# Performance work log

Hardware: AMD Instinct MI355X
Metric: run time of the kernel (lower is better)

The kernel has to match this reference:

```python
import jax, jax.numpy as jnp
import numpy as np

N = 50000
E = 800000
IN_CH = 256
HID = 64
HEADS = 8
OUT_CH = 16
NEG_SLOPE = 0.2


def _glorot(key, shape):
    fan_in, fan_out = shape[0], shape[-1]
    lim = float(np.sqrt(6.0 / (fan_in + fan_out)))
    return jax.random.uniform(key, shape, jnp.float32, -lim, lim)


def setup_inputs() -> dict:
    key = jax.random.key(0)
    ks = jax.random.split(key, 12)
    x = jax.random.normal(ks[0], (N, IN_CH), jnp.float32)
    edge_index = jax.random.randint(ks[1], (2, E), 0, N, jnp.int64)
    # layer 1: GATConv(256 -> 64, heads=8)
    W1 = _glorot(ks[2], (IN_CH, HEADS * HID))
    a_src1 = _glorot(ks[3], (HEADS, HID))
    a_dst1 = _glorot(ks[4], (HEADS, HID))
    b1 = jnp.zeros((HEADS * HID,), jnp.float32)
    # layer 2: GATConv(512 -> 16, heads=1, concat=False)
    W2 = _glorot(ks[5], (HEADS * HID, OUT_CH))
    a_src2 = _glorot(ks[6], (1, OUT_CH))
    a_dst2 = _glorot(ks[7], (1, OUT_CH))
    b2 = jnp.zeros((OUT_CH,), jnp.float32)
    return {"x": x, "edge_index": edge_index, "W1": W1, "a_src1": a_src1,
            "a_dst1": a_dst1, "b1": b1, "W2": W2, "a_src2": a_src2,
            "a_dst2": a_dst2, "b2": b2}


def _gat_conv(x, src, dst, W, a_src, a_dst, bias, heads, out_ch, concat):
    n = x.shape[0]
    h = (x @ W).reshape(n, heads, out_ch)            # [N,H,C]
    alpha_s = jnp.einsum('nhc,hc->nh', h, a_src)      # [N,H]
    alpha_d = jnp.einsum('nhc,hc->nh', h, a_dst)
    e = alpha_s[src] + alpha_d[dst]                   # [E,H]
    e = jnp.where(e > 0, e, NEG_SLOPE * e)            # leaky_relu
    # segment softmax over incoming edges of each dst node
    e_max = jax.ops.segment_max(e, dst, num_segments=n)
    e_max = jnp.where(jnp.isfinite(e_max), e_max, 0.0)
    p = jnp.exp(e - e_max[dst])                       # [E,H]
    denom = jax.ops.segment_sum(p, dst, num_segments=n)
    alpha = p / (denom[dst] + 1e-16)                  # [E,H]
    msg = h[src] * alpha[:, :, None]                  # [E,H,C]
    out = jax.ops.segment_sum(msg, dst, num_segments=n)  # [N,H,C]
    if concat:
        out = out.reshape(n, heads * out_ch)
    else:
        out = out.mean(axis=1)
    return out + bias


def reference(x, edge_index, W1, a_src1, a_dst1, b1, W2, a_src2, a_dst2, b2):
    n = x.shape[0]
    loops = jnp.arange(n, dtype=edge_index.dtype)
    ei = jnp.concatenate([edge_index, jnp.stack([loops, loops])], axis=1)
    src, dst = ei[0], ei[1]
    h = _gat_conv(x, src, dst, W1, a_src1, a_dst1, b1, HEADS, HID, True)
    h = jax.nn.elu(h)
    out = _gat_conv(h, src, dst, W2, a_src2, a_dst2, b2, 1, OUT_CH, False)
    return jax.nn.log_softmax(out, axis=-1)
```

## Files before the change

kernel.cpp:

```cpp
#include <hip/hip_runtime.h>
#include <math.h>

#define IN_CH 256
#define HID 64
#define HEADS 8
#define F1 512
#define OUT_CH 16
#define NEG 0.2f

typedef __attribute__((ext_vector_type(8))) short bf16x8;
typedef __attribute__((ext_vector_type(4))) float f32x4;
typedef __attribute__((ext_vector_type(2))) float f32x2;

__device__ __forceinline__ unsigned short f2bf(float f) {
  unsigned int u = __builtin_bit_cast(unsigned int, f);
  u += 0x7FFFu + ((u >> 16) & 1u);
  return (unsigned short)(u >> 16);
}
__device__ __forceinline__ void gld_lds16(const void* g, void* l) {
  __builtin_amdgcn_global_load_lds(
      (const __attribute__((address_space(1))) unsigned int*)g,
      (__attribute__((address_space(3))) unsigned int*)l, 16, 0, 0);
}


__global__ void prep_kernel(const int* __restrict__ ei, int E, int N,
                            int* counts,
                            const float* __restrict__ W1, unsigned short* __restrict__ W1R,
                            const float* __restrict__ W2, unsigned short* __restrict__ W2T) {
  int idx = blockIdx.x * blockDim.x + threadIdx.x;
  int ET = E + N;
  if (idx < ET) {
    int dst = (idx < E) ? ei[E + idx] : (idx - E);
    atomicAdd(&counts[dst], 1);
  }
  if (idx < F1 * IN_CH) {
    int n = idx >> 8, k = idx & 255;
    int r = (((k >> 5) * 4 + ((k >> 3) & 3)) * 512 + n) * 8 + (k & 7);
    W1R[r] = f2bf(W1[k * F1 + n]);
  }
  if (idx < OUT_CH * F1) {
    int n = idx >> 9, k = idx & 511;
    W2T[idx] = f2bf(W2[k * OUT_CH + n]);
  }
}


__global__ __launch_bounds__(1024) void scan_kernel(const int* __restrict__ counts,
                                                    int* __restrict__ offsets,
                                                    int* __restrict__ bsum,
                                                    int* bars, int n) {
  __shared__ int lds[1024];
  __shared__ int s_pre, s_tot;
  int nb = gridDim.x;
  int t = threadIdx.x;
  int i = blockIdx.x * 1024 + t;
  int v = (i < n) ? counts[i] : 0;
  lds[t] = v;
  __syncthreads();
  for (int off = 1; off < 1024; off <<= 1) {
    int u = (t >= off) ? lds[t - off] : 0;
    __syncthreads();
    lds[t] += u;
    __syncthreads();
  }
  int incl = lds[t];
  if (t == 1023) bsum[blockIdx.x] = incl;
  __syncthreads();
  if (t == 0) {
    __threadfence();
    atomicAdd(&bars[0], 1);
    while (atomicAdd(&bars[0], 0) < nb) __builtin_amdgcn_s_sleep(8);
  }
  __syncthreads();
  if (t < 64) {
    int bv = (t < nb) ? bsum[t] : 0;
    int vp = (t < (int)blockIdx.x) ? bv : 0;
    #pragma unroll
    for (int off = 1; off < 64; off <<= 1) {
      vp += __shfl_xor(vp, off);
      bv += __shfl_xor(bv, off);
    }
    if (t == 0) { s_pre = vp; s_tot = bv; }
  }
  __syncthreads();
  if (i < n) offsets[i] = s_pre + incl - v;
  if (blockIdx.x == 0 && t == 0) offsets[n] = s_tot;
}

__global__ void fill_kernel(const int* __restrict__ ei, int E, int N,
                            const int* __restrict__ offsets, int* cursor,
                            int* __restrict__ csr_src) {
  int e = blockIdx.x * blockDim.x + threadIdx.x;
  int ET = E + N;
  if (e >= ET) return;
  int src, dst;
  if (e < E) { src = ei[e]; dst = ei[E + e]; }
  else       { src = e - E; dst = e - E; }
  int pos = atomicAdd(&cursor[dst], 1);
  csr_src[offsets[dst] + pos] = src;
}


__global__ __launch_bounds__(512) void gemm1_mfma(const float* __restrict__ X,
                                                  const unsigned short* __restrict__ W1R,
                                                  const float* __restrict__ Asrc,
                                                  const float* __restrict__ Adst,
                                                  unsigned char* __restrict__ C,
                                                  float2* __restrict__ aad1, int M) {
  __shared__ __align__(16) short sB[4 * 512 * 8];
  int tid = threadIdx.x, w = tid >> 6, l = tid & 63;
  int wm = (w >> 2) * 32;
  int wn = (w & 3) * 128;
  int bm = blockIdx.x * 64;
  f32x4 acc[2][8];
  #pragma unroll
  for (int mi = 0; mi < 2; ++mi)
    #pragma unroll
    for (int nj = 0; nj < 8; ++nj) acc[mi][nj] = (f32x4){0.f, 0.f, 0.f, 0.f};
  int kslot = l >> 4;
  for (int kb = 0; kb < 8; ++kb) {
    __syncthreads();
    const unsigned short* src = W1R + kb * 16384;
    #pragma unroll
    for (int i = 0; i < 4; ++i)
      gld_lds16(src + (size_t)(i * 512 + tid) * 8, (char*)sB + (i * 512 + tid) * 16);
    bf16x8 af[2];
    int kbase = kb * 32 + kslot * 8;
    #pragma unroll
    for (int mi = 0; mi < 2; ++mi) {
      int r = bm + wm + mi * 16 + (l & 15);
      if (r >= M) r = M - 1;
      const float* ap = X + (size_t)r * IN_CH + kbase;
      float4 a0 = *(const float4*)ap;
      float4 a1 = *(const float4*)(ap + 4);
      unsigned int u0, u1, u2, u3;
      asm("v_cvt_pk_bf16_f32 %0, %1, %2" : "=v"(u0) : "v"(a0.x), "v"(a0.y));
      asm("v_cvt_pk_bf16_f32 %0, %1, %2" : "=v"(u1) : "v"(a0.z), "v"(a0.w));
      asm("v_cvt_pk_bf16_f32 %0, %1, %2" : "=v"(u2) : "v"(a1.x), "v"(a1.y));
      asm("v_cvt_pk_bf16_f32 %0, %1, %2" : "=v"(u3) : "v"(a1.z), "v"(a1.w));
      int4 pk = make_int4(u0, u1, u2, u3);
      af[mi] = __builtin_bit_cast(bf16x8, pk);
    }
    __syncthreads();
    #pragma unroll
    for (int nj = 0; nj < 8; ++nj) {
      int n = wn + nj * 16 + (l & 15);
      bf16x8 bf = *(const bf16x8*)&sB[(kslot * 512 + n) * 8];
      acc[0][nj] = __builtin_amdgcn_mfma_f32_16x16x32_bf16(af[0], bf, acc[0][nj], 0, 0, 0);
      acc[1][nj] = __builtin_amdgcn_mfma_f32_16x16x32_bf16(af[1], bf, acc[1][nj], 0, 0, 0);
    }
  }
  float asv[8], adv[8];
  #pragma unroll
  for (int nj = 0; nj < 8; ++nj) {
    int c = wn + nj * 16 + (l & 15);
    asv[nj] = Asrc[c]; adv[nj] = Adst[c];
  }
  int h0 = (w & 3) * 2;
  #pragma unroll
  for (int mi = 0; mi < 2; ++mi) {
    #pragma unroll
    for (int j = 0; j < 4; ++j) {
      int r = bm + wm + mi * 16 + (l >> 4) * 4 + j;
      bool ok = (r < M);
      if (ok) {
        #pragma unroll
        for (int njp = 0; njp < 4; ++njp) {
          int u = __builtin_amdgcn_cvt_pk_fp8_f32(acc[mi][2 * njp][j],
                                                  acc[mi][2 * njp + 1][j], 0, false);
          int c0 = wn + (2 * njp) * 16 + (l & 15);
          C[(size_t)r * F1 + c0]      = (unsigned char)u;
          C[(size_t)r * F1 + c0 + 16] = (unsigned char)(u >> 8);
        }
      }
      float sA = 0.f, dA = 0.f, sB2 = 0.f, dB2 = 0.f;
      #pragma unroll
      for (int nj = 0; nj < 4; ++nj) {
        float v = acc[mi][nj][j];
        sA += v * asv[nj]; dA += v * adv[nj];
      }
      #pragma unroll
      for (int nj = 4; nj < 8; ++nj) {
        float v = acc[mi][nj][j];
        sB2 += v * asv[nj]; dB2 += v * adv[nj];
      }
      #pragma unroll
      for (int off = 1; off < 16; off <<= 1) {
        sA += __shfl_xor(sA, off); dA += __shfl_xor(dA, off);
        sB2 += __shfl_xor(sB2, off); dB2 += __shfl_xor(dB2, off);
      }
      if (ok && (l & 15) == 0) {
        aad1[r * HEADS + h0]     = make_float2(sA, dA);
        aad1[r * HEADS + h0 + 1] = make_float2(sB2, dB2);
      }
    }
  }
}


__global__ __launch_bounds__(256) void aggr1_kernel(const uint2* __restrict__ h1q,
                                                    const float2* __restrict__ aad1,
                                                    const int* __restrict__ offsets,
                                                    const int* __restrict__ csr_src,
                                                    const float* __restrict__ b1,
                                                    uint4* __restrict__ out1v, int N) {
  int tid = threadIdx.x;
  int w = tid >> 6, l = tid & 63;
  int b = blockIdx.x;
  int nwg = gridDim.x;
  int q = nwg >> 3, r = nwg & 7;
  int xcd = b & 7, bi = b >> 3;
  int swz = (xcd < r) ? (xcd * (q + 1) + bi) : (r * (q + 1) + (xcd - r) * q + bi);
  int node = swz * 4 + w;
  if (node >= N) return;
  int beg = offsets[node], deg = offsets[node + 1] - beg;
  int he = l & 7;
  int hc = l >> 3;
  float adv = aad1[node * HEADS + he].y;
  float pden = 0.f;
  f32x2 acc2[4];
  #pragma unroll
  for (int i = 0; i < 4; ++i) acc2[i] = (f32x2){0.f, 0.f};
  int e = l >> 3;
  for (int c0 = 0; c0 < deg; c0 += 8) {
    int cnt = min(8, deg - c0);
    int s8 = 0;
    float p8 = 0.f;
    if (e < cnt) {
      s8 = csr_src[beg + c0 + e];
      float2 sd = aad1[s8 * HEADS + he];
      float ev = sd.x + adv;
      ev = (ev > 0.f) ? ev : NEG * ev;
      p8 = __expf(ev);
      pden += p8;
    }
    if (cnt == 8) {
      int ss[8]; float qq[8];
      #pragma unroll
      for (int j = 0; j < 8; ++j) {
        ss[j] = __shfl(s8, j * 8);
        qq[j] = __shfl(p8, j * 8 + hc);
      }
      uint2 v[8];
      #pragma unroll
      for (int j = 0; j < 8; ++j) v[j] = h1q[(size_t)ss[j] * 64 + l];
      #pragma unroll
      for (int j = 0; j < 8; ++j) {
        f32x2 p2 = (f32x2){qq[j], qq[j]};
        acc2[0] += p2 * __builtin_amdgcn_cvt_pk_f32_fp8(v[j].x, false);
        acc2[1] += p2 * __builtin_amdgcn_cvt_pk_f32_fp8(v[j].x, true);
        acc2[2] += p2 * __builtin_amdgcn_cvt_pk_f32_fp8(v[j].y, false);
        acc2[3] += p2 * __builtin_amdgcn_cvt_pk_f32_fp8(v[j].y, true);
      }
    } else {
      for (int j = 0; j < cnt; ++j) {
        int s = __shfl(s8, j * 8);
        float p = __shfl(p8, j * 8 + hc);
        uint2 v = h1q[(size_t)s * 64 + l];
        f32x2 p2 = (f32x2){p, p};
        acc2[0] += p2 * __builtin_amdgcn_cvt_pk_f32_fp8(v.x, false);
        acc2[1] += p2 * __builtin_amdgcn_cvt_pk_f32_fp8(v.x, true);
        acc2[2] += p2 * __builtin_amdgcn_cvt_pk_f32_fp8(v.y, false);
        acc2[3] += p2 * __builtin_amdgcn_cvt_pk_f32_fp8(v.y, true);
      }
    }
  }
  pden += __shfl_xor(pden, 8);
  pden += __shfl_xor(pden, 16);
  pden += __shfl_xor(pden, 32);
  float den = __shfl(pden, hc) + 1e-16f;
  float4 bv0 = *(const float4*)&b1[l * 8];
  float4 bv1 = *(const float4*)&b1[l * 8 + 4];
  float o[8];
  o[0] = acc2[0][0] / den + bv0.x; o[1] = acc2[0][1] / den + bv0.y;
  o[2] = acc2[1][0] / den + bv0.z; o[3] = acc2[1][1] / den + bv0.w;
  o[4] = acc2[2][0] / den + bv1.x; o[5] = acc2[2][1] / den + bv1.y;
  o[6] = acc2[3][0] / den + bv1.z; o[7] = acc2[3][1] / den + bv1.w;
  #pragma unroll
  for (int i = 0; i < 8; ++i) o[i] = (o[i] > 0.f) ? o[i] : expm1f(o[i]);
  uint4 ov;
  ov.x = (unsigned int)f2bf(o[0]) | ((unsigned int)f2bf(o[1]) << 16);
  ov.y = (unsigned int)f2bf(o[2]) | ((unsigned int)f2bf(o[3]) << 16);
  ov.z = (unsigned int)f2bf(o[4]) | ((unsigned int)f2bf(o[5]) << 16);
  ov.w = (unsigned int)f2bf(o[6]) | ((unsigned int)f2bf(o[7]) << 16);
  out1v[(size_t)node * 64 + l] = ov;
}


__global__ __launch_bounds__(256) void gemm2_mfma(const unsigned short* __restrict__ A,
                                                  const unsigned short* __restrict__ W2T,
                                                  const float* __restrict__ a_src2,
                                                  const float* __restrict__ a_dst2,
                                                  float* __restrict__ t2,
                                                  float2* __restrict__ aad2, int M) {
  __shared__ __align__(16) short sW[16 * 512];
  int tid = threadIdx.x, w = tid >> 6, l = tid & 63;
  for (int i = tid; i < 1024; i += 256) ((uint4*)sW)[i] = ((const uint4*)W2T)[i];
  __syncthreads();
  int bm = blockIdx.x * 128 + w * 32;
  f32x4 acc[2];
  acc[0] = (f32x4){0.f, 0.f, 0.f, 0.f};
  acc[1] = (f32x4){0.f, 0.f, 0.f, 0.f};
  int rl = l & 15;
  int koff = (l >> 4) * 8;
  int r0 = bm + rl;       if (r0 >= M) r0 = M - 1;
  int r1 = bm + 16 + rl;  if (r1 >= M) r1 = M - 1;
  const unsigned short* a0p = A + (size_t)r0 * F1 + koff;
  const unsigned short* a1p = A + (size_t)r1 * F1 + koff;
  #pragma unroll
  for (int k0 = 0; k0 < F1; k0 += 32) {
    bf16x8 bfv = *(const bf16x8*)&sW[rl * 512 + k0 + koff];
    bf16x8 af0 = *(const bf16x8*)(a0p + k0);
    bf16x8 af1 = *(const bf16x8*)(a1p + k0);
    acc[0] = __builtin_amdgcn_mfma_f32_16x16x32_bf16(af0, bfv, acc[0], 0, 0, 0);
    acc[1] = __builtin_amdgcn_mfma_f32_16x16x32_bf16(af1, bfv, acc[1], 0, 0, 0);
  }
  float asv = a_src2[rl], adv = a_dst2[rl];
  #pragma unroll
  for (int mi = 0; mi < 2; ++mi) {
    #pragma unroll
    for (int j = 0; j < 4; ++j) {
      int r = bm + mi * 16 + (l >> 4) * 4 + j;
      float val = acc[mi][j];
      float s = val * asv, d = val * adv;
      s += __shfl_xor(s, 1); s += __shfl_xor(s, 2); s += __shfl_xor(s, 4); s += __shfl_xor(s, 8);
      d += __shfl_xor(d, 1); d += __shfl_xor(d, 2); d += __shfl_xor(d, 4); d += __shfl_xor(d, 8);
      if (r < M) {
        t2[(size_t)r * OUT_CH + rl] = val;
        if (rl == 0) aad2[r] = make_float2(s, d);
      }
    }
  }
}


__global__ __launch_bounds__(256) void aggr2_kernel(const float* __restrict__ t2,
                                                    const float2* __restrict__ aad2,
                                                    const int* __restrict__ offsets,
                                                    const int* __restrict__ csr_src,
                                                    const float* __restrict__ b2,
                                                    float* __restrict__ out, int N) {
  int tid = threadIdx.x;
  int node = blockIdx.x * 4 + (tid >> 6);
  int lane = tid & 63;
  if (node >= N) return;
  int beg = offsets[node];
  int deg = offsets[node + 1] - beg;
  float ad = aad2[node].y;
  float acc = 0.f, den = 0.f;
  int eg = lane >> 4, c = lane & 15;
  for (int base = 0; base < deg; base += 8) {
    int j1 = base + eg;
    int j2 = base + 4 + eg;
    bool ok1 = j1 < deg, ok2 = j2 < deg;
    int s1 = csr_src[beg + (ok1 ? j1 : 0)];
    int s2 = csr_src[beg + (ok2 ? j2 : 0)];
    float2 m1 = aad2[s1];
    float2 m2 = aad2[s2];
    float t1v = t2[(size_t)s1 * OUT_CH + c];
    float t2v = t2[(size_t)s2 * OUT_CH + c];
    float e1 = m1.x + ad;
    e1 = (e1 > 0.f) ? e1 : NEG * e1;
    float p1 = ok1 ? __expf(e1) : 0.f;
    float e2 = m2.x + ad;
    e2 = (e2 > 0.f) ? e2 : NEG * e2;
    float p2 = ok2 ? __expf(e2) : 0.f;
    acc += p1 * t1v + p2 * t2v;
    if (c == 0) den += p1 + p2;
  }
  acc += __shfl_xor(acc, 16); acc += __shfl_xor(acc, 32);
  den += __shfl_xor(den, 16); den += __shfl_xor(den, 32);
  den = __shfl(den, 0);
  float val = acc / (den + 1e-16f) + b2[c];
  float mx = val;
  #pragma unroll
  for (int off = 1; off < 16; off <<= 1) mx = fmaxf(mx, __shfl_xor(mx, off));
  float ex = __expf(val - mx);
  float se = ex;
  #pragma unroll
  for (int off = 1; off < 16; off <<= 1) se += __shfl_xor(se, off);
  float ls = val - mx - logf(se);
  if (lane < 16) out[(size_t)node * OUT_CH + lane] = ls;
}


extern "C" void kernel_launch(void* const* d_in, const int* in_sizes, int n_in,
                              void* d_out, int out_size, void* d_ws, size_t ws_size,
                              hipStream_t stream) {
  const float* x      = (const float*)d_in[0];
  const int*   ei     = (const int*)d_in[1];
  const float* W1     = (const float*)d_in[2];
  const float* a_src1 = (const float*)d_in[3];
  const float* a_dst1 = (const float*)d_in[4];
  const float* b1     = (const float*)d_in[5];
  const float* W2     = (const float*)d_in[6];
  const float* a_src2 = (const float*)d_in[7];
  const float* a_dst2 = (const float*)d_in[8];
  const float* b2     = (const float*)d_in[9];
  float* out = (float*)d_out;

  int N = in_sizes[0] / IN_CH;
  int E = in_sizes[1] / 2;
  int ET = E + N;

  char* w = (char*)d_ws;
  auto alloc = [&](size_t bytes) -> void* {
    void* p = (void*)w;
    w += (bytes + 255) & ~(size_t)255;
    return p;
  };
  unsigned char*  h1b   = (unsigned char*)alloc((size_t)N * F1);
  unsigned short* out1b = (unsigned short*)alloc((size_t)N * F1 * 2);
  unsigned short* w1r   = (unsigned short*)alloc((size_t)F1 * IN_CH * 2);
  unsigned short* w2t   = (unsigned short*)alloc((size_t)OUT_CH * F1 * 2);
  float* aad1  = (float*)alloc((size_t)N * HEADS * 8);
  float* t2    = (float*)alloc((size_t)N * OUT_CH * 4);
  float* aad2  = (float*)alloc((size_t)N * 8);
  int* counts  = (int*)alloc((size_t)N * 2 * 4 + 256);
  int* cursor  = counts + N;
  int* bars    = counts + 2 * N;
  int* offsets = (int*)alloc((size_t)(N + 1) * 4);
  int* bsum    = (int*)alloc(256 * 4);
  int* csr_src = (int*)alloc((size_t)ET * 4);

  int nb = (N + 1023) / 1024;

  hipMemsetAsync(counts, 0, (size_t)N * 2 * 4 + 256, stream);
  prep_kernel<<<(ET + 255) / 256, 256, 0, stream>>>(ei, E, N, counts, W1, w1r, W2, w2t);
  scan_kernel<<<nb, 1024, 0, stream>>>(counts, offsets, bsum, bars, N);
  fill_kernel<<<(ET + 255) / 256, 256, 0, stream>>>(ei, E, N, offsets, cursor, csr_src);

  gemm1_mfma<<<(N + 63) / 64, 512, 0, stream>>>(x, w1r, a_src1, a_dst1, h1b,
                                                (float2*)aad1, N);
  aggr1_kernel<<<(N + 3) / 4, 256, 0, stream>>>((const uint2*)h1b, (const float2*)aad1,
                                                offsets, csr_src, b1, (uint4*)out1b, N);
  gemm2_mfma<<<(N + 127) / 128, 256, 0, stream>>>(out1b, w2t, a_src2, a_dst2, t2,
                                                  (float2*)aad2, N);
  aggr2_kernel<<<(N + 3) / 4, 256, 0, stream>>>(t2, (const float2*)aad2, offsets, csr_src,
                                                b2, out, N);
}
```

Baseline: 265.3 us.

## Fuse CSR build stages into one persistent kernel with grid barriers

Merges the count/prep, scan and fill kernels plus most of the memset into a single persistent kernel of 256 blocks × 1024 threads, separated by software grid-wide barriers. Counter zeroing moves into the kernel, and only the barrier counters are memset. This removes several launch gaps and a large memset. It relies on all 256 blocks being co-resident; if they are not, the spin barriers deadlock. The atomics and scatter phases also run with fewer threads in grid-stride loops.

After: 315.7 us. 1.19x slower.

```diff
diff --git a/kernel.cpp b/kernel.cpp
--- a/kernel.cpp
+++ b/kernel.cpp
@@ -23,82 +23,96 @@
       (__attribute__((address_space(3))) unsigned int*)l, 16, 0, 0);
 }
 
-
-__global__ void prep_kernel(const int* __restrict__ ei, int E, int N,
-                            int* counts,
-                            const float* __restrict__ W1, unsigned short* __restrict__ W1R,
-                            const float* __restrict__ W2, unsigned short* __restrict__ W2T) {
-  int idx = blockIdx.x * blockDim.x + threadIdx.x;
+__device__ __forceinline__ void gbar(int* ctr, int nb) {
+  __syncthreads();
+  if (threadIdx.x == 0) {
+    __threadfence();
+    atomicAdd(ctr, 1);
+    while (atomicAdd(ctr, 0) < nb) __builtin_amdgcn_s_sleep(8);
+  }
+  __syncthreads();
+}
+
+
+__global__ __launch_bounds__(1024) void build_kernel(const int* __restrict__ ei, int E, int N,
+                                                     int* counts, int* cursor,
+                                                     int* __restrict__ offsets,
+                                                     int* __restrict__ bsum,
+                                                     int* __restrict__ csr_src,
+                                                     const float* __restrict__ W1,
+                                                     unsigned short* __restrict__ W1R,
+                                                     const float* __restrict__ W2,
+                                                     unsigned short* __restrict__ W2T,
+                                                     int* bars) {
+  int nb = gridDim.x;
+  int t = threadIdx.x;
+  int gid = blockIdx.x * 1024 + t;
+  int stride = nb * 1024;
   int ET = E + N;
-  if (idx < ET) {
-    int dst = (idx < E) ? ei[E + idx] : (idx - E);
+  __shared__ int lds[1024];
+  __shared__ int s_pre, s_tot;
+
+  for (int i = gid; i < N; i += stride) { counts[i] = 0; cursor[i] = 0; }
+  gbar(&bars[0], nb);
+
+  for (int e = gid; e < ET; e += stride) {
+    int dst = (e < E) ? ei[E + e] : (e - E);
     atomicAdd(&counts[dst], 1);
   }
-  if (idx < F1 * IN_CH) {
+  for (int idx = gid; idx < F1 * IN_CH; idx += stride) {
     int n = idx >> 8, k = idx & 255;
     int r = (((k >> 5) * 4 + ((k >> 3) & 3)) * 512 + n) * 8 + (k & 7);
     W1R[r] = f2bf(W1[k * F1 + n]);
   }
-  if (idx < OUT_CH * F1) {
+  for (int idx = gid; idx < OUT_CH * F1; idx += stride) {
     int n = idx >> 9, k = idx & 511;
     W2T[idx] = f2bf(W2[k * OUT_CH + n]);
   }
-}
-
-
-__global__ __launch_bounds__(1024) void scan_kernel(const int* __restrict__ counts,
-                                                    int* __restrict__ offsets,
-                                                    int* __restrict__ bsum,
-                                                    int* bars, int n) {
-  __shared__ int lds[1024];
-  __shared__ int s_pre, s_tot;
-  int nb = gridDim.x;
-  int t = threadIdx.x;
-  int i = blockIdx.x * 1024 + t;
-  int v = (i < n) ? counts[i] : 0;
-  lds[t] = v;
-  __syncthreads();
-  for (int off = 1; off < 1024; off <<= 1) {
-    int u = (t >= off) ? lds[t - off] : 0;
+  gbar(&bars[1], nb);
+
+  int nscan = (N + 1023) / 1024;
+  int incl = 0, v = 0;
+  if ((int)blockIdx.x < nscan) {
+    int i = blockIdx.x * 1024 + t;
+    v = (i < N) ? counts[i] : 0;
+    lds[t] = v;
     __syncthreads();
-    lds[t] += u;
+    for (int off = 1; off < 1024; off <<= 1) {
+      int u = (t >= off) ? lds[t - off] : 0;
+      __syncthreads();
+      lds[t] += u;
+      __syncthreads();
+    }
+    incl = lds[t];
+    if (t == 1023) bsum[blockIdx.x] = incl;
+  }
+  gbar(&bars[2], nb);
+
+  if ((int)blockIdx.x < nscan) {
+    if (t < 64) {
+      int bv = (t < nscan) ? bsum[t] : 0;
+      int vp = (t < (int)blockIdx.x) ? bv : 0;
+      #pragma unroll
+      for (int off = 1; off < 64; off <<= 1) {
+        vp += __shfl_xor(vp, off);
+        bv += __shfl_xor(bv, off);
+      }
+      if (t == 0) { s_pre = vp; s_tot = bv; }
+    }
     __syncthreads();
-  }
-  int incl = lds[t];
-  if (t == 1023) bsum[blockIdx.x] = incl;
-  __syncthreads();
-  if (t == 0) {
-    __threadfence();
-    atomicAdd(&bars[0], 1);
-    while (atomicAdd(&bars[0], 0) < nb) __builtin_amdgcn_s_sleep(8);
-  }
-  __syncthreads();
-  if (t < 64) {
-    int bv = (t < nb) ? bsum[t] : 0;
-    int vp = (t < (int)blockIdx.x) ? bv : 0;
-    #pragma unroll
-    for (int off = 1; off < 64; off <<= 1) {
-      vp += __shfl_xor(vp, off);
-      bv += __shfl_xor(bv, off);
-    }
-    if (t == 0) { s_pre = vp; s_tot = bv; }
-  }
-  __syncthreads();
-  if (i < n) offsets[i] = s_pre + incl - v;
-  if (blockIdx.x == 0 && t == 0) offsets[n] = s_tot;
-}
-
-__global__ void fill_kernel(const int* __restrict__ ei, int E, int N,
-                            const int* __restrict__ offsets, int* cursor,
-                            int* __restrict__ csr_src) {
-  int e = blockIdx.x * blockDim.x + threadIdx.x;
-  int ET = E + N;
-  if (e >= ET) return;
-  int src, dst;
-  if (e < E) { src = ei[e]; dst = ei[E + e]; }
-  else       { src = e - E; dst = e - E; }
-  int pos = atomicAdd(&cursor[dst], 1);
-  csr_src[offsets[dst] + pos] = src;
+    int i = blockIdx.x * 1024 + t;
+    if (i < N) offsets[i] = s_pre + incl - v;
+    if (blockIdx.x == 0 && t == 0) offsets[N] = s_tot;
+  }
+  gbar(&bars[3], nb);
+
+  for (int e = gid; e < ET; e += stride) {
+    int src, dst;
+    if (e < E) { src = ei[e]; dst = ei[E + e]; }
+    else       { src = e - E; dst = e - E; }
+    int pos = atomicAdd(&cursor[dst], 1);
+    csr_src[offsets[dst] + pos] = src;
+  }
 }
 
 
@@ -417,20 +431,16 @@
   float* aad1  = (float*)alloc((size_t)N * HEADS * 8);
   float* t2    = (float*)alloc((size_t)N * OUT_CH * 4);
   float* aad2  = (float*)alloc((size_t)N * 8);
-  int* counts  = (int*)alloc((size_t)N * 2 * 4 + 256);
+  int* counts  = (int*)alloc((size_t)N * 2 * 4);
   int* cursor  = counts + N;
-  int* bars    = counts + 2 * N;
+  int* bars    = (int*)alloc(256);
   int* offsets = (int*)alloc((size_t)(N + 1) * 4);
   int* bsum    = (int*)alloc(256 * 4);
   int* csr_src = (int*)alloc((size_t)ET * 4);
 
-  int nb = (N + 1023) / 1024;
-
-  hipMemsetAsync(counts, 0, (size_t)N * 2 * 4 + 256, stream);
-  prep_kernel<<<(ET + 255) / 256, 256, 0, stream>>>(ei, E, N, counts, W1, w1r, W2, w2t);
-  scan_kernel<<<nb, 1024, 0, stream>>>(counts, offsets, bsum, bars, N);
-  fill_kernel<<<(ET + 255) / 256, 256, 0, stream>>>(ei, E, N, offsets, cursor, csr_src);
-
+  hipMemsetAsync(bars, 0, 256, stream);
+  build_kernel<<<256, 1024, 0, stream>>>(ei, E, N, counts, cursor, offsets, bsum, csr_src,
+                                         W1, w1r, W2, w2t, bars);
   gemm1_mfma<<<(N + 63) / 64, 512, 0, stream>>>(x, w1r, a_src1, a_dst1, h1b,
                                                 (float2*)aad1, N);
   aggr1_kernel<<<(N + 3) / 4, 256, 0, stream>>>((const uint2*)h1b, (const float2*)aad1,
```
